# Kernel optimization log

Hardware: AMD Instinct MI355X
Metric: run time of the kernel (lower is better)

The kernel has to match this reference:

```python
import jax, jax.numpy as jnp
import numpy as np

# Static hyperparams matching init_kwargs
KSIZE, STRIDE, PAD, DIL = 3, 2, 1, 1


def setup_inputs() -> dict:
    key = jax.random.key(0)
    k1, k2 = jax.random.split(key)
    B, H, W, Cin, Cout = 8, 128, 128, 128, 256
    feats = jax.random.normal(k1, (B * H * W, Cin), dtype=jnp.float32)
    weight = jax.random.normal(k2, (KSIZE * KSIZE, Cin, Cout), dtype=jnp.float32) * 0.05
    alpha_upper = jnp.ones((1,), dtype=jnp.float32)
    # dense grid coords [N, 3] = (batch, y, x), matching a dense image sparse tensor
    bb, yy, xx = np.meshgrid(np.arange(B), np.arange(H), np.arange(W), indexing='ij')
    coords = jnp.asarray(np.stack([bb, yy, xx], -1).reshape(-1, 3), dtype=jnp.int32)
    return {"feats": feats, "weight": weight, "alpha_upper": alpha_upper,
            "coords": coords, "H": H, "W": W, "B": B}


def _coord_ranges(H, W):
    # Faithful translation of WrappedMinkowskiStridedOperation.__init__ + forward
    # coordinate math, specialized to a dense grid (per-batch min=0, max=H-1/W-1).
    kernel_origin = DIL * ((KSIZE - 1) // 2) * (KSIZE % 2)
    dilated = DIL * (KSIZE - 1) + 1
    ks_off = kernel_origin - dilated + 1          # _kernel_start_offset
    ke_off = kernel_origin                        # _kernel_end_offset
    idx_start = kernel_origin - PAD               # _index_start_offset
    ranges = []
    for ext in (H, W):
        idx_end = (ext - 1) + kernel_origin + PAD - dilated + 2
        start = max(idx_start, (0 + ks_off - idx_start) // STRIDE * STRIDE + idx_start)
        end = min(idx_end, ((ext - 1 + ke_off - idx_start) // STRIDE + 1) * STRIDE + idx_start)
        ranges.append(np.arange(start, end, STRIDE))
    offsets = np.arange(KSIZE) * DIL - kernel_origin  # kernel region offsets
    return ranges[0], ranges[1], offsets, idx_start


def reference(feats, weight, alpha_upper, coords, H, W, B):
    Cin = feats.shape[1]
    Cout = weight.shape[-1]
    ys, xs, offs, idx_start = _coord_ranges(H, W)
    OH, OW = len(ys), len(xs)
    oy, ox = jnp.meshgrid(jnp.asarray(ys, jnp.int32), jnp.asarray(xs, jnp.int32), indexing='ij')
    dy, dx = np.meshgrid(offs, offs, indexing='ij')
    dy = jnp.asarray(dy.reshape(-1), jnp.int32)  # [kvol]
    dx = jnp.asarray(dx.reshape(-1), jnp.int32)
    ny = oy[None] + dy[:, None, None]            # [kvol, OH, OW]
    nx = ox[None] + dx[:, None, None]
    valid = (ny >= 0) & (ny < H) & (nx >= 0) & (nx < W)
    lin = jnp.clip(ny, 0, H - 1) * W + jnp.clip(nx, 0, W - 1)  # [kvol, OH, OW]
    feats3 = feats.reshape(B, H * W, Cin)
    gathered = feats3[:, lin]                    # [B, kvol, OH, OW, Cin]
    gathered = jnp.where(valid[None, ..., None], gathered, jnp.zeros((), feats.dtype))
    out = jnp.einsum('bkhwc,kcd->bhwd', gathered, weight)  # [B, OH, OW, Cout]
    out_feats = out.reshape(B * OH * OW, Cout)
    # output coordinates, remapped as in forward (shift by index_start, divide by stride)
    oc = jnp.stack([oy, ox], -1).reshape(-1, 2)  # [OH*OW, 2]
    oc = (oc - jnp.int32(idx_start)) // jnp.int32(STRIDE)
    oc = jnp.tile(oc, (B, 1))
    bcol = jnp.repeat(jnp.arange(B, dtype=jnp.int32), OH * OW)
    out_coords = jnp.concatenate([bcol[:, None], oc], axis=1)
    return out_feats, out_coords, alpha_upper
```

## Files before the change

### kernel.cpp

```cpp
#include <hip/hip_runtime.h>


#define OUT_FEATS_ELEMS (32768 * 256)
#define OUT_COORDS_OFF  OUT_FEATS_ELEMS
#define ALPHA_OFF       (OUT_FEATS_ELEMS + 32768 * 3)

#define BW_BYTES   (18 * 16384)

typedef float v16f __attribute__((ext_vector_type(16)));

__device__ __forceinline__ unsigned pk4fp8(float a, float b, float c, float d) {
    unsigned u = 0;
    u = __builtin_amdgcn_cvt_pk_fp8_f32(a, b, u, false);
    u = __builtin_amdgcn_cvt_pk_fp8_f32(c, d, u, true);
    return u;
}

#define GLOAD_LDS16(SRC, DST)                                                  \
    __builtin_amdgcn_global_load_lds(                                          \
        (const __attribute__((address_space(1))) void*)(SRC),                  \
        (__attribute__((address_space(3))) void*)(DST), 16, 0, 0)

__global__ void wprep_kernel(const float* __restrict__ w,
                             const float* __restrict__ alpha,
                             unsigned char* __restrict__ Bw,
                             float* __restrict__ out) {
    int cid = blockIdx.x * 256 + threadIdx.x;
    if (cid < 32768) {
        int b = cid >> 12, iy = (cid >> 6) & 63, ix = cid & 63;
        float* c = out + OUT_COORDS_OFF + (size_t)cid * 3;
        c[0] = (float)b; c[1] = (float)iy; c[2] = (float)ix;
        if (cid == 0) out[ALPHA_OFF] = alpha[0];
    }
    if (cid < 18432) {
        int ch  = cid & 7;
        int row = (cid >> 3) & 127;
        int t   = cid >> 10;
        int nb  = (t >= 9) ? 1 : 0;
        int tap = t - 9 * nb;
        int chp = ch ^ (row & 7);
        int n   = (nb << 7) + row;
        int kb  = (tap << 7) + (chp << 4);
        unsigned u[4];
#pragma unroll
        for (int q = 0; q < 4; ++q) {
            float f0 = w[(size_t)(kb + 4 * q + 0) * 256 + n];
            float f1 = w[(size_t)(kb + 4 * q + 1) * 256 + n];
            float f2 = w[(size_t)(kb + 4 * q + 2) * 256 + n];
            float f3 = w[(size_t)(kb + 4 * q + 3) * 256 + n];
            u[q] = pk4fp8(f0, f1, f2, f3);
        }
        uint4 r; r.x = u[0]; r.y = u[1]; r.z = u[2]; r.w = u[3];
        *(uint4*)(Bw + (size_t)cid * 16) = r;
    }
}

__global__ void coords_alpha_kernel(float* __restrict__ out, const float* __restrict__ alpha) {
    int i = blockIdx.x * 256 + threadIdx.x;
    int b = i >> 12, iy = (i >> 6) & 63, ix = i & 63;
    float* c = out + OUT_COORDS_OFF + (size_t)i * 3;
    c[0] = (float)b; c[1] = (float)iy; c[2] = (float)ix;
    if (i == 0) out[ALPHA_OFF] = alpha[0];
}

__global__ __launch_bounds__(512, 1) void gemm_conv_kernel(
    const float* __restrict__ feats,
    const unsigned char* __restrict__ Bw,
    float* __restrict__ out)
{
    __shared__ unsigned char Aband[5 * 130 * 128];
    __shared__ unsigned char Bs[2][256 * 128];

    const int tid  = threadIdx.x;
    const int bid  = blockIdx.x;
    const int my   = ((bid & 7) << 5) + (bid >> 3);
    const int m0   = my << 7;
    const int bb   = my >> 5;
    const int iy0  = ((my & 31) << 1);

    const int lane = tid & 63, wave = tid >> 6;
    const int wm   = (wave >> 2) << 6;
    const int wn   = (wave & 3) << 6;
    const int l31  = lane & 31;
    const int hh   = lane >> 5;
    const int xorl = l31 & 7;

    if (tid < 40) {
        const int r = tid >> 3, c = tid & 7;
        uint4 z; z.x = 0u; z.y = 0u; z.z = 0u; z.w = 0u;
        *(uint4*)(Aband + ((r * 130) << 7) + (c << 4)) = z;
    }
    if (iy0 == 0) {
        for (int z = tid; z < 1040; z += 512) {
            const int nxp = z >> 3, c = z & 7;
            uint4 zz; zz.x = 0u; zz.y = 0u; zz.z = 0u; zz.w = 0u;
            *(uint4*)(Aband + (nxp << 7) + ((c ^ ((nxp >> 1) & 7)) << 4)) = zz;
        }
    }

    {
        const int vstart = (iy0 == 0) ? 1 : 0;
        const int iters  = (5 - vstart) << 3;
        const int ny0    = (iy0 << 1) - 1;
        for (int it = 0; it < iters; ++it) {
            const int o   = (tid + (it << 9)) << 4;
            const int r   = vstart + (o >> 16);
            const int br  = o & 65535;
            const int nx  = br >> 9;
            const int ch0 = (br & 511) >> 2;
            const float4 f = *(const float4*)(feats +
                ((((size_t)(bb << 14) + (ny0 + r) * 128 + nx)) << 7) + ch0);
            const unsigned u = pk4fp8(f.x, f.y, f.z, f.w);
            const int c   = ch0 >> 4;
            const int nxp = nx + 1;
            *(unsigned*)(Aband + ((r * 130 + nxp) << 7)
                         + ((c ^ ((nxp >> 1) & 7)) << 4) + (ch0 & 15)) = u;
        }
    }
    __syncthreads();

    const unsigned char* bsrc0 = Bw + ((size_t)((wave >> 2) * 9) << 14)
                                    + ((size_t)(wave & 3) << 12) + ((size_t)lane << 4);
    auto stageB = [&](int tap, int buf) {
        const unsigned char* bs = bsrc0 + ((size_t)tap << 14);
        unsigned char* bdst = Bs[buf] + (wave << 12);
#pragma unroll
        for (int q = 0; q < 4; ++q)
            GLOAD_LDS16(bs + (q << 10), bdst + (q << 10));
    };

    v16f acc[2][2];
#pragma unroll
    for (int i = 0; i < 2; i++)
#pragma unroll
        for (int j = 0; j < 2; j++) acc[i][j] = (v16f)(0.0f);

    auto computeTap = [&](int buf, int dy, int dx) {
        const int bandrow = (wm >> 5) + dy + 1;
        int abase[2], akey[2];
#pragma unroll
        for (int i = 0; i < 2; ++i) {
            const int ixv = (i << 5) + l31;
            const int nxp = (ixv << 1) + dx + 1;
            abase[i] = ((bandrow * 130 + nxp) << 7) + (hh << 3);
            akey[i]  = (nxp >> 1) & 7;
        }
#pragma unroll
        for (int seg = 0; seg < 8; ++seg) {
            long long a[2], b2[2];
#pragma unroll
            for (int i = 0; i < 2; i++)
                a[i] = *(const long long*)(Aband + abase[i] + ((seg ^ akey[i]) << 4));
#pragma unroll
            for (int j = 0; j < 2; j++)
                b2[j] = *(const long long*)(Bs[buf] + ((wn + (j << 5) + l31) << 7)
                                            + ((seg ^ xorl) << 4) + (hh << 3));
            __builtin_amdgcn_s_setprio(1);
#pragma unroll
            for (int i = 0; i < 2; i++)
#pragma unroll
                for (int j = 0; j < 2; j++)
                    acc[i][j] = __builtin_amdgcn_mfma_f32_32x32x16_fp8_fp8(a[i], b2[j], acc[i][j], 0, 0, 0);
            __builtin_amdgcn_s_setprio(0);
        }
    };

    stageB(0, 0);

#pragma unroll
    for (int tap = 0; tap < 9; ++tap) {
        if (tap < 8) {
            stageB(tap + 1, (tap + 1) & 1);
            asm volatile("s_waitcnt vmcnt(4)\ns_barrier" ::: "memory");
        } else {
            asm volatile("s_waitcnt vmcnt(0)\ns_barrier" ::: "memory");
        }
        computeTap(tap & 1, tap / 3 - 1, tap % 3 - 1);
        if (tap < 8)
            asm volatile("s_barrier" ::: "memory");
    }

#pragma unroll
    for (int i = 0; i < 2; i++)
#pragma unroll
        for (int j = 0; j < 2; j++) {
            const int gcol = wn + (j << 5) + l31;
#pragma unroll
            for (int r = 0; r < 16; ++r) {
                const int grow = m0 + wm + (i << 5) + (r & 3) + ((r >> 2) << 3) + (hh << 2);
                __builtin_nontemporal_store(acc[i][j][r], &out[(size_t)grow * 256 + gcol]);
            }
        }
}

__global__ void naive_conv_kernel(const float* __restrict__ feats,
                                  const float* __restrict__ w,
                                  float* __restrict__ out) {
    int m = blockIdx.x;
    int n = threadIdx.x;
    int bb = m >> 12, iy = (m >> 6) & 63, ix = m & 63;
    float acc = 0.f;
    for (int tap = 0; tap < 9; ++tap) {
        int ny = 2 * iy + tap / 3 - 1;
        int nx = 2 * ix + tap % 3 - 1;
        if ((unsigned)ny < 128u && (unsigned)nx < 128u) {
            const float* fr = feats + ((size_t)((bb << 14) + (ny << 7) + nx) << 7);
            const float* wr = w + tap * 32768 + n;
            for (int c = 0; c < 128; ++c) acc += fr[c] * wr[c * 256];
        }
    }
    out[(size_t)m * 256 + n] = acc;
}

extern "C" void kernel_launch(void* const* d_in, const int* in_sizes, int n_in,
                              void* d_out, int out_size, void* d_ws, size_t ws_size,
                              hipStream_t stream) {
    const float* feats  = (const float*)d_in[0];
    const float* weight = (const float*)d_in[1];
    const float* alpha  = (const float*)d_in[2];
    float* out = (float*)d_out;

    const size_t NEED = (size_t)BW_BYTES;
    if (ws_size >= NEED) {
        unsigned char* Bw = (unsigned char*)d_ws;
        wprep_kernel<<<144, 256, 0, stream>>>(weight, alpha, Bw, out);
        gemm_conv_kernel<<<256, 512, 0, stream>>>(feats, Bw, out);
    } else {
        coords_alpha_kernel<<<128, 256, 0, stream>>>(out, alpha);
        naive_conv_kernel<<<32768, 256, 0, stream>>>(feats, weight, out);
    }
}
```

Baseline: 132.4 us.

## Double threads per block to 1024 with smaller per-wave tiles

The conv GEMM block grows from 8 to 16 waves, and each wave now computes a 32x128 output tile instead of 64x128, with two accumulators in place of four. The band load and B staging are split across more threads, and the first B tap prefetch is issued before the A band conversion so the two overlap. The aim is more latency hiding and parallelism in the fp8-conversion band load and the MFMA loop. The cost is less A/B register reuse per wave and more LDS reads per MFMA.

```diff
diff --git a/kernel.cpp b/kernel.cpp
--- a/kernel.cpp
+++ b/kernel.cpp
@@ -63,7 +63,7 @@
     if (i == 0) out[ALPHA_OFF] = alpha[0];
 }
 
-__global__ __launch_bounds__(512, 1) void gemm_conv_kernel(
+__global__ __launch_bounds__(1024, 1) void gemm_conv_kernel(
     const float* __restrict__ feats,
     const unsigned char* __restrict__ Bw,
     float* __restrict__ out)
@@ -79,19 +79,31 @@
     const int iy0  = ((my & 31) << 1);
 
     const int lane = tid & 63, wave = tid >> 6;
-    const int wm   = (wave >> 2) << 6;
+    const int wm   = (wave >> 2) << 5;
     const int wn   = (wave & 3) << 6;
     const int l31  = lane & 31;
     const int hh   = lane >> 5;
     const int xorl = l31 & 7;
 
+    const unsigned char* bsrc0 = Bw + ((size_t)((wave >> 3) * 9) << 14)
+                                    + ((size_t)(wave & 7) << 11) + ((size_t)lane << 4);
+    auto stageB = [&](int tap, int buf) {
+        const unsigned char* bs = bsrc0 + ((size_t)tap << 14);
+        unsigned char* bdst = Bs[buf] + (wave << 11);
+#pragma unroll
+        for (int q = 0; q < 2; ++q)
+            GLOAD_LDS16(bs + (q << 10), bdst + (q << 10));
+    };
+
+    stageB(0, 0);
+
     if (tid < 40) {
         const int r = tid >> 3, c = tid & 7;
         uint4 z; z.x = 0u; z.y = 0u; z.z = 0u; z.w = 0u;
         *(uint4*)(Aband + ((r * 130) << 7) + (c << 4)) = z;
     }
     if (iy0 == 0) {
-        for (int z = tid; z < 1040; z += 512) {
+        for (int z = tid; z < 1040; z += 1024) {
             const int nxp = z >> 3, c = z & 7;
             uint4 zz; zz.x = 0u; zz.y = 0u; zz.z = 0u; zz.w = 0u;
             *(uint4*)(Aband + (nxp << 7) + ((c ^ ((nxp >> 1) & 7)) << 4)) = zz;
@@ -99,79 +111,59 @@
     }
 
     {
-        const int vstart = (iy0 == 0) ? 1 : 0;
-        const int iters  = (5 - vstart) << 3;
-        const int ny0    = (iy0 << 1) - 1;
-        for (int it = 0; it < iters; ++it) {
-            const int o   = (tid + (it << 9)) << 4;
-            const int r   = vstart + (o >> 16);
-            const int br  = o & 65535;
-            const int nx  = br >> 9;
-            const int ch0 = (br & 511) >> 2;
-            const float4 f = *(const float4*)(feats +
-                ((((size_t)(bb << 14) + (ny0 + r) * 128 + nx)) << 7) + ch0);
-            const unsigned u = pk4fp8(f.x, f.y, f.z, f.w);
-            const int c   = ch0 >> 4;
-            const int nxp = nx + 1;
-            *(unsigned*)(Aband + ((r * 130 + nxp) << 7)
-                         + ((c ^ ((nxp >> 1) & 7)) << 4) + (ch0 & 15)) = u;
-        }
+        const int ny0 = (iy0 << 1) - 1;
+        auto loadBand = [&](int vstart, int iters) {
+#pragma unroll 4
+            for (int it = 0; it < iters; ++it) {
+                const int o   = (tid + (it << 10)) << 4;
+                const int r   = vstart + (o >> 16);
+                const int br  = o & 65535;
+                const int nx  = br >> 9;
+                const int ch0 = (br & 511) >> 2;
+                const float4 f = *(const float4*)(feats +
+                    ((((size_t)(bb << 14) + (ny0 + r) * 128 + nx)) << 7) + ch0);
+                const unsigned u = pk4fp8(f.x, f.y, f.z, f.w);
+                const int c   = ch0 >> 4;
+                const int nxp = nx + 1;
+                *(unsigned*)(Aband + ((r * 130 + nxp) << 7)
+                             + ((c ^ ((nxp >> 1) & 7)) << 4) + (ch0 & 15)) = u;
+            }
+        };
+        if (iy0 == 0) loadBand(1, 16); else loadBand(0, 20);
     }
     __syncthreads();
 
-    const unsigned char* bsrc0 = Bw + ((size_t)((wave >> 2) * 9) << 14)
-                                    + ((size_t)(wave & 3) << 12) + ((size_t)lane << 4);
-    auto stageB = [&](int tap, int buf) {
-        const unsigned char* bs = bsrc0 + ((size_t)tap << 14);
-        unsigned char* bdst = Bs[buf] + (wave << 12);
-#pragma unroll
-        for (int q = 0; q < 4; ++q)
-            GLOAD_LDS16(bs + (q << 10), bdst + (q << 10));
-    };
-
-    v16f acc[2][2];
-#pragma unroll
-    for (int i = 0; i < 2; i++)
-#pragma unroll
-        for (int j = 0; j < 2; j++) acc[i][j] = (v16f)(0.0f);
+    v16f acc[2];
+#pragma unroll
+    for (int j = 0; j < 2; j++) acc[j] = (v16f)(0.0f);
 
     auto computeTap = [&](int buf, int dy, int dx) {
-        const int bandrow = (wm >> 5) + dy + 1;
-        int abase[2], akey[2];
-#pragma unroll
-        for (int i = 0; i < 2; ++i) {
-            const int ixv = (i << 5) + l31;
-            const int nxp = (ixv << 1) + dx + 1;
-            abase[i] = ((bandrow * 130 + nxp) << 7) + (hh << 3);
-            akey[i]  = (nxp >> 1) & 7;
-        }
+        const int bandrow = ((wm >> 6) << 1) + dy + 1;
+        const int ixv = (wm & 63) + l31;
+        const int nxp = (ixv << 1) + dx + 1;
+        const int abase = ((bandrow * 130 + nxp) << 7) + (hh << 3);
+        const int akey  = (nxp >> 1) & 7;
 #pragma unroll
         for (int seg = 0; seg < 8; ++seg) {
-            long long a[2], b2[2];
-#pragma unroll
-            for (int i = 0; i < 2; i++)
-                a[i] = *(const long long*)(Aband + abase[i] + ((seg ^ akey[i]) << 4));
+            long long a0, b2[2];
+            a0 = *(const long long*)(Aband + abase + ((seg ^ akey) << 4));
 #pragma unroll
             for (int j = 0; j < 2; j++)
                 b2[j] = *(const long long*)(Bs[buf] + ((wn + (j << 5) + l31) << 7)
                                             + ((seg ^ xorl) << 4) + (hh << 3));
             __builtin_amdgcn_s_setprio(1);
 #pragma unroll
-            for (int i = 0; i < 2; i++)
-#pragma unroll
-                for (int j = 0; j < 2; j++)
-                    acc[i][j] = __builtin_amdgcn_mfma_f32_32x32x16_fp8_fp8(a[i], b2[j], acc[i][j], 0, 0, 0);
+            for (int j = 0; j < 2; j++)
+                acc[j] = __builtin_amdgcn_mfma_f32_32x32x16_fp8_fp8(a0, b2[j], acc[j], 0, 0, 0);
             __builtin_amdgcn_s_setprio(0);
         }
     };
-
-    stageB(0, 0);
 
 #pragma unroll
     for (int tap = 0; tap < 9; ++tap) {
         if (tap < 8) {
             stageB(tap + 1, (tap + 1) & 1);
-            asm volatile("s_waitcnt vmcnt(4)\ns_barrier" ::: "memory");
+            asm volatile("s_waitcnt vmcnt(2)\ns_barrier" ::: "memory");
         } else {
             asm volatile("s_waitcnt vmcnt(0)\ns_barrier" ::: "memory");
         }
@@ -181,16 +173,14 @@
     }
 
 #pragma unroll
-    for (int i = 0; i < 2; i++)
-#pragma unroll
-        for (int j = 0; j < 2; j++) {
-            const int gcol = wn + (j << 5) + l31;
-#pragma unroll
-            for (int r = 0; r < 16; ++r) {
-                const int grow = m0 + wm + (i << 5) + (r & 3) + ((r >> 2) << 3) + (hh << 2);
-                __builtin_nontemporal_store(acc[i][j][r], &out[(size_t)grow * 256 + gcol]);
-            }
-        }
+    for (int j = 0; j < 2; j++) {
+        const int gcol = wn + (j << 5) + l31;
+#pragma unroll
+        for (int r = 0; r < 16; ++r) {
+            const int grow = m0 + wm + (r & 3) + ((r >> 2) << 3) + (hh << 2);
+            __builtin_nontemporal_store(acc[j][r], &out[(size_t)grow * 256 + gcol]);
+        }
+    }
 }
 
 __global__ void naive_conv_kernel(const float* __restrict__ feats,
@@ -224,7 +214,7 @@
     if (ws_size >= NEED) {
         unsigned char* Bw = (unsigned char*)d_ws;
         wprep_kernel<<<144, 256, 0, stream>>>(weight, alpha, Bw, out);
-        gemm_conv_kernel<<<256, 512, 0, stream>>>(feats, Bw, out);
+        gemm_conv_kernel<<<256, 1024, 0, stream>>>(feats, Bw, out);
     } else {
         coords_alpha_kernel<<<128, 256, 0, stream>>>(out, alpha);
         naive_conv_kernel<<<32768, 256, 0, stream>>>(feats, weight, out);
```

Result: no change. 132.7 us (+0.3%).

## Overlap A-band row loads with tap compute and add half-swizzle to LDS layout

Applied to the files above, without the earlier changes.

Stops loading the full 5-row activation band before any MFMA work. Only rows 0 and 2 are loaded up front, and rows 1, 3 and 4 are issued into registers and written to LDS between taps, interleaved with the weight staging using hand-tuned vmcnt waits. It also adds an extra XOR swizzle on the 8-byte half within each 16-byte segment, for both the A band and the prepacked weights, to reduce LDS bank conflicts on the 8-byte reads. The manual waitcnt counts are fragile, raise register pressure through the float4 staging arrays, and any miscount can produce wrong data.

```diff
diff --git a/kernel.cpp b/kernel.cpp
--- a/kernel.cpp
+++ b/kernel.cpp
@@ -20,6 +20,11 @@
     __builtin_amdgcn_global_load_lds(                                          \
         (const __attribute__((address_space(1))) void*)(SRC),                  \
         (__attribute__((address_space(3))) void*)(DST), 16, 0, 0)
+
+#define WAITBAR_(N) asm volatile("s_waitcnt vmcnt(" #N ")\n\ts_barrier" ::: "memory")
+#define WAITBAR(N)  WAITBAR_(N)
+#define BAR()       asm volatile("s_barrier" ::: "memory")
+#define LGKMBAR()   asm volatile("s_waitcnt lgkmcnt(0)\n\ts_barrier" ::: "memory")
 
 __global__ void wprep_kernel(const float* __restrict__ w,
                              const float* __restrict__ alpha,
@@ -39,15 +44,17 @@
         int nb  = (t >= 9) ? 1 : 0;
         int tap = t - 9 * nb;
         int chp = ch ^ (row & 7);
+        int hb  = (row >> 3) & 1;
         int n   = (nb << 7) + row;
         int kb  = (tap << 7) + (chp << 4);
         unsigned u[4];
 #pragma unroll
         for (int q = 0; q < 4; ++q) {
-            float f0 = w[(size_t)(kb + 4 * q + 0) * 256 + n];
-            float f1 = w[(size_t)(kb + 4 * q + 1) * 256 + n];
-            float f2 = w[(size_t)(kb + 4 * q + 2) * 256 + n];
-            float f3 = w[(size_t)(kb + 4 * q + 3) * 256 + n];
+            int kq = kb + 4 * (q ^ (hb << 1));
+            float f0 = w[(size_t)(kq + 0) * 256 + n];
+            float f1 = w[(size_t)(kq + 1) * 256 + n];
+            float f2 = w[(size_t)(kq + 2) * 256 + n];
+            float f3 = w[(size_t)(kq + 3) * 256 + n];
             u[q] = pk4fp8(f0, f1, f2, f3);
         }
         uint4 r; r.x = u[0]; r.y = u[1]; r.z = u[2]; r.w = u[3];
@@ -84,40 +91,7 @@
     const int l31  = lane & 31;
     const int hh   = lane >> 5;
     const int xorl = l31 & 7;
-
-    if (tid < 40) {
-        const int r = tid >> 3, c = tid & 7;
-        uint4 z; z.x = 0u; z.y = 0u; z.z = 0u; z.w = 0u;
-        *(uint4*)(Aband + ((r * 130) << 7) + (c << 4)) = z;
-    }
-    if (iy0 == 0) {
-        for (int z = tid; z < 1040; z += 512) {
-            const int nxp = z >> 3, c = z & 7;
-            uint4 zz; zz.x = 0u; zz.y = 0u; zz.z = 0u; zz.w = 0u;
-            *(uint4*)(Aband + (nxp << 7) + ((c ^ ((nxp >> 1) & 7)) << 4)) = zz;
-        }
-    }
-
-    {
-        const int vstart = (iy0 == 0) ? 1 : 0;
-        const int iters  = (5 - vstart) << 3;
-        const int ny0    = (iy0 << 1) - 1;
-        for (int it = 0; it < iters; ++it) {
-            const int o   = (tid + (it << 9)) << 4;
-            const int r   = vstart + (o >> 16);
-            const int br  = o & 65535;
-            const int nx  = br >> 9;
-            const int ch0 = (br & 511) >> 2;
-            const float4 f = *(const float4*)(feats +
-                ((((size_t)(bb << 14) + (ny0 + r) * 128 + nx)) << 7) + ch0);
-            const unsigned u = pk4fp8(f.x, f.y, f.z, f.w);
-            const int c   = ch0 >> 4;
-            const int nxp = nx + 1;
-            *(unsigned*)(Aband + ((r * 130 + nxp) << 7)
-                         + ((c ^ ((nxp >> 1) & 7)) << 4) + (ch0 & 15)) = u;
-        }
-    }
-    __syncthreads();
+    const int bhalf = (hh ^ ((l31 >> 3) & 1)) << 3;
 
     const unsigned char* bsrc0 = Bw + ((size_t)((wave >> 2) * 9) << 14)
                                     + ((size_t)(wave & 3) << 12) + ((size_t)lane << 4);
@@ -129,6 +103,54 @@
             GLOAD_LDS16(bs + (q << 10), bdst + (q << 10));
     };
 
+    const int ny0 = (iy0 << 1) - 1;
+    auto issueRow = [&](int r, float4* f) {
+        const int ny = ny0 + r;
+#pragma unroll
+        for (int it = 0; it < 8; ++it) {
+            const int idx = (it << 9) + tid;
+            const int nx  = idx >> 5;
+            const int c4  = (idx & 31) << 2;
+            f[it] = *(const float4*)(feats +
+                ((((size_t)(bb << 14) + ny * 128 + nx)) << 7) + c4);
+        }
+    };
+    auto writeRow = [&](int r, const float4* f) {
+#pragma unroll
+        for (int it = 0; it < 8; ++it) {
+            const int idx = (it << 9) + tid;
+            const int nx  = idx >> 5;
+            const int c4  = (idx & 31) << 2;
+            const unsigned u = pk4fp8(f[it].x, f[it].y, f[it].z, f[it].w);
+            const int nxp  = nx + 1;
+            const int key4 = (nxp >> 1) & 15;
+            const int boff = ((r * 130 + nxp) << 7)
+                + (((c4 >> 4) ^ (key4 & 7)) << 4)
+                + (((((c4 >> 3) & 1) ^ (key4 >> 3)) & 1) << 3)
+                + (c4 & 7);
+            *(unsigned*)(Aband + boff) = u;
+        }
+    };
+
+    stageB(0, 0);
+    if (tid < 40) {
+        const int r = tid >> 3, c = tid & 7;
+        uint4 z; z.x = 0u; z.y = 0u; z.z = 0u; z.w = 0u;
+        *(uint4*)(Aband + ((r * 130) << 7) + (c << 4)) = z;
+    }
+    if (iy0 == 0) {
+        for (int z = tid; z < 1040; z += 512) {
+            uint4 zz; zz.x = 0u; zz.y = 0u; zz.z = 0u; zz.w = 0u;
+            *(uint4*)(Aband + z * 16) = zz;
+        }
+    }
+    float4 fA[8], fB[8];
+    if (iy0 > 0) issueRow(0, fA);
+    issueRow(2, fB);
+    if (iy0 > 0) writeRow(0, fA);
+    writeRow(2, fB);
+    __syncthreads();
+
     v16f acc[2][2];
 #pragma unroll
     for (int i = 0; i < 2; i++)
@@ -137,24 +159,25 @@
 
     auto computeTap = [&](int buf, int dy, int dx) {
         const int bandrow = (wm >> 5) + dy + 1;
-        int abase[2], akey[2];
+        int abase[2], kc[2];
 #pragma unroll
         for (int i = 0; i < 2; ++i) {
-            const int ixv = (i << 5) + l31;
-            const int nxp = (ixv << 1) + dx + 1;
-            abase[i] = ((bandrow * 130 + nxp) << 7) + (hh << 3);
-            akey[i]  = (nxp >> 1) & 7;
+            const int ixv  = (i << 5) + l31;
+            const int nxp  = (ixv << 1) + dx + 1;
+            const int key4 = (nxp >> 1) & 15;
+            abase[i] = ((bandrow * 130 + nxp) << 7) + ((hh ^ (key4 >> 3)) << 3);
+            kc[i]    = key4 & 7;
         }
 #pragma unroll
         for (int seg = 0; seg < 8; ++seg) {
             long long a[2], b2[2];
 #pragma unroll
             for (int i = 0; i < 2; i++)
-                a[i] = *(const long long*)(Aband + abase[i] + ((seg ^ akey[i]) << 4));
+                a[i] = *(const long long*)(Aband + abase[i] + ((seg ^ kc[i]) << 4));
 #pragma unroll
             for (int j = 0; j < 2; j++)
                 b2[j] = *(const long long*)(Bs[buf] + ((wn + (j << 5) + l31) << 7)
-                                            + ((seg ^ xorl) << 4) + (hh << 3));
+                                            + ((seg ^ xorl) << 4) + bhalf);
             __builtin_amdgcn_s_setprio(1);
 #pragma unroll
             for (int i = 0; i < 2; i++)
@@ -165,20 +188,29 @@
         }
     };
 
-    stageB(0, 0);
-
-#pragma unroll
-    for (int tap = 0; tap < 9; ++tap) {
-        if (tap < 8) {
-            stageB(tap + 1, (tap + 1) & 1);
-            asm volatile("s_waitcnt vmcnt(4)\ns_barrier" ::: "memory");
-        } else {
-            asm volatile("s_waitcnt vmcnt(0)\ns_barrier" ::: "memory");
-        }
-        computeTap(tap & 1, tap / 3 - 1, tap % 3 - 1);
-        if (tap < 8)
-            asm volatile("s_barrier" ::: "memory");
-    }
+    stageB(1, 1); issueRow(1, fA); issueRow(3, fB);
+    BAR();
+    computeTap(0, -1, -1); BAR();
+    stageB(2, 0); WAITBAR(20);
+    computeTap(1, -1, 0); BAR();
+    stageB(3, 1); WAITBAR(4);
+    computeTap(0, -1, 1);
+    writeRow(1, fA); writeRow(3, fB);
+    LGKMBAR();
+    stageB(4, 0); issueRow(4, fA); WAITBAR(12);
+    computeTap(1, 0, -1); BAR();
+    stageB(5, 1); WAITBAR(12);
+    computeTap(0, 0, 0); BAR();
+    stageB(6, 0); WAITBAR(4);
+    computeTap(1, 0, 1);
+    writeRow(4, fA);
+    LGKMBAR();
+    stageB(7, 1); WAITBAR(4);
+    computeTap(0, 1, -1); BAR();
+    stageB(8, 0); WAITBAR(4);
+    computeTap(1, 1, 0); BAR();
+    WAITBAR(0);
+    computeTap(0, 1, 1);
 
 #pragma unroll
     for (int i = 0; i < 2; i++)
```

After: 128.1 us. -3.2%, faster.
